# Kernel optimization log

Hardware: AMD Instinct MI355X
Metric: run time of the kernel (lower is better)

The kernel has to match this reference:

```python
import jax, jax.numpy as jnp
import numpy as np


def sparsemax(z):
    # sparsemax along the last axis (matches tfa.activations.sparsemax default axis=-1)
    K = z.shape[-1]
    zs = -jnp.sort(-z, axis=-1)                      # descending sort
    cs = jnp.cumsum(zs, axis=-1)
    k = jnp.arange(1, K + 1, dtype=z.dtype)
    support = 1.0 + k * zs > cs                      # support set indicator
    kmax = jnp.sum(support, axis=-1, keepdims=True)  # |support|, int
    cs_k = jnp.take_along_axis(cs, kmax - 1, axis=-1)
    tau = (cs_k - 1.0) / kmax.astype(z.dtype)
    return jnp.maximum(z - tau, 0.0)


def binary_lut(depth):
    # (depth, 2**depth, 2) table mapping leaf index -> per-level bit / complement
    idx = np.arange(2 ** depth)
    off = 2 ** np.arange(depth)
    bits = (idx[None, :] // off[:, None]) % 2        # (depth, 2**depth)
    return jnp.asarray(np.stack([bits, 1 - bits], axis=-1), dtype=jnp.float32)


def setup_inputs() -> dict:
    key = jax.random.key(0)
    ks = jax.random.split(key, 5)
    B, F, N, D, U = 8192, 256, 128, 6, 16
    return {
        "x": jax.random.normal(ks[0], (B, F), dtype=jnp.float32),
        "feature_selection_logits": jax.random.normal(ks[1], (F, N, D), dtype=jnp.float32),
        "feature_thresholds": jax.random.normal(ks[2], (N, D), dtype=jnp.float32),
        "log_temperatures": jax.random.normal(ks[3], (N, D), dtype=jnp.float32) * 0.1,
        "response": jax.random.normal(ks[4], (N, U, 2 ** D), dtype=jnp.float32),
        "depth": D,
    }


def reference(x, feature_selection_logits, feature_thresholds, log_temperatures, response, depth):
    lut = binary_lut(depth)                                          # (d, 2**d, 2)
    selectors = sparsemax(feature_selection_logits)                  # (i, n, d)
    fv = jnp.einsum('bi,ind->bnd', x, selectors)                     # (b, n, d)
    tl = (fv - feature_thresholds) * jnp.exp(-log_temperatures)      # (b, n, d)
    tl = jnp.stack([-tl, tl], axis=-1)                               # (b, n, d, 2)
    gates = jnp.clip(0.5 * tl + 0.5, 0.0, 1.0)                       # sparsemoid
    rg = jnp.einsum('bnds,dcs->bndc', gates, lut)                    # (b, n, d, 2**d)
    rg = jnp.prod(rg, axis=-2)                                       # (b, n, 2**d)
    resp = jnp.einsum('bnc,nuc->bnu', rg, response)                  # (b, n, u)
    return jnp.mean(resp, axis=1)                                    # (b, u)
```

## Files before the change

### kernel.cpp

```cpp
#include <hip/hip_runtime.h>


typedef float f32x4 __attribute__((ext_vector_type(4)));
typedef unsigned int u32;
typedef _Float16 h16;
typedef _Float16 h16x2 __attribute__((ext_vector_type(2)));
typedef _Float16 h16x8 __attribute__((ext_vector_type(8)));

typedef unsigned short __attribute__((may_alias)) u16a;
typedef u32            __attribute__((may_alias)) u32a;
typedef float          __attribute__((may_alias)) f32a;

#define WPF_OFF   0
#define RESPF_OFF 393216
#define BIAS_OFF  655360

union h2u { h16x2 h; u32 u; };
union hbits { h16 h; unsigned short s; };
union fragh { u32 w[4]; h16x8 v; int4 i4; h16x2 h2[4]; };

__device__ inline unsigned short h16r(float f) {
    hbits t; t.h = (h16)f; return t.s;
}
__device__ inline u32 packh2(float a, float b) {
    h2u t; t.h[0] = (h16)a; t.h[1] = (h16)b; return t.u;
}

__device__ inline f32x4 mfma_f16(h16x8 a, h16x8 b, f32x4 c) {
    return __builtin_amdgcn_mfma_f32_16x16x32_f16(a, b, c, 0, 0, 0);
}

__global__ __launch_bounds__(256) void k_prep(const float* __restrict__ fsl,
                                              const float* __restrict__ thr,
                                              const float* __restrict__ logt,
                                              const float* __restrict__ resp,
                                              unsigned short* __restrict__ WpF,
                                              unsigned short* __restrict__ respF,
                                              float* __restrict__ bias) {
    int bb  = blockIdx.x;
    int tid = threadIdx.x;
    if (bb < 128) {
        __shared__ unsigned short sm[8][192];
        int ib = (bb & 31) * 8;
        int nb = (bb >> 5) * 32;
        int il = tid >> 5;
        int nl = tid & 31;
        int i = ib + il;
        int n = nb + nl;
        const float* zp = fsl + (i * 128 + n) * 6;

        float z[6], zs[6];
        #pragma unroll
        for (int d = 0; d < 6; ++d) { z[d] = zp[d]; zs[d] = z[d]; }
        #pragma unroll
        for (int a = 0; a < 5; ++a) {
            #pragma unroll
            for (int b = a + 1; b < 6; ++b) {
                float hi = fmaxf(zs[a], zs[b]);
                float lo = fminf(zs[a], zs[b]);
                zs[a] = hi; zs[b] = lo;
            }
        }
        float cs = 0.f, csel = 0.f;
        int   km = 1;
        #pragma unroll
        for (int k = 0; k < 6; ++k) {
            cs += zs[k];
            if (1.0f + (float)(k + 1) * zs[k] > cs) { km = k + 1; csel = cs; }
        }
        float tau = (csel - 1.0f) / (float)km;

        #pragma unroll
        for (int d = 0; d < 6; ++d) {
            float invT = expf(-logt[n * 6 + d]);
            float sel  = fmaxf(z[d] - tau, 0.0f);
            float wv   = sel * 0.5f * invT;
            sm[il][nl * 6 + d] = h16r(wv);
            if (i == 0) bias[n * 6 + d] = 0.5f - 0.5f * invT * thr[n * 6 + d];
        }
        __syncthreads();

        if (tid < 192) {
            int ct  = (nb * 6) / 16 + (tid >> 4);
            int clm = tid & 15;
            int kt  = ib >> 5;
            int lq  = (ib >> 3) & 3;
            union { unsigned short s[8]; int4 i4; } o;
            #pragma unroll
            for (int j = 0; j < 8; ++j) o.s[j] = sm[j][tid];
            *(int4*)(WpF + (size_t)(((ct * 8 + kt) * 64 + lq * 16 + clm) * 8)) = o.i4;
        }
    } else {
        int t = (bb - 128) * 256 + tid;
        int n  = t >> 7;
        int k2 = (t >> 6) & 1;
        int l  = t & 63;
        int u  = l & 15;
        int c0 = k2 * 32 + (l >> 4) * 8;
        const float* rp = resp + n * 1024 + u * 64 + c0;
        float4 ra = *(const float4*)rp;
        float4 rb = *(const float4*)(rp + 4);
        int4 o;
        o.x = (int)packh2(ra.x, ra.y);
        o.y = (int)packh2(ra.z, ra.w);
        o.z = (int)packh2(rb.x, rb.y);
        o.w = (int)packh2(rb.z, rb.w);
        ((int4*)respF)[(n * 2 + k2) * 64 + l] = o;
    }
}

__global__ __launch_bounds__(1024, 4) void k_main(const float* __restrict__ x,
                                                  const unsigned short* __restrict__ WpF,
                                                  const unsigned short* __restrict__ respF,
                                                  const float* __restrict__ bias,
                                                  float* __restrict__ out) {
    __shared__ char smemraw[65536];
    const int4* xf4 = (const int4*)smemraw;

    int tid = threadIdx.x;
    int w  = tid >> 6;
    int l  = tid & 63;
    int cl = l & 15;
    int lq = l >> 4;
    int rowbase = blockIdx.x * 32;
    int ctbase  = w * 3;

    u16a* gw = (u16a*)(smemraw + 16384 + w * 3072);
    const int4* wp4 = (const int4*)WpF;
    const int4* rp4 = (const int4*)respF;

    {
        int k8  = tid & 31;
        int row = tid >> 5;
        const float* xp = x + (size_t)(rowbase + row) * 256 + k8 * 8;
        float4 xa = *(const float4*)(xp);
        float4 xb = *(const float4*)(xp + 4);
        int4 p;
        p.x = (int)packh2(xa.x, xa.y);
        p.y = (int)packh2(xa.z, xa.w);
        p.z = (int)packh2(xb.x, xb.y);
        p.w = (int)packh2(xb.z, xb.w);
        int rt = row >> 4, rl = row & 15, kt = k8 >> 2, klq = k8 & 3;
        char* basep = smemraw + (size_t)(rt * 8 + kt) * 1024
                              + (size_t)(((klq * 16 + rl) ^ kt) * 16);
        *(int4*)basep = p;
    }

    fragh bc[3];
    #pragma unroll
    for (int j = 0; j < 3; ++j)
        bc[j].i4 = wp4[((ctbase + j) * 8 + 0) * 64 + l];

    __syncthreads();

    f32x4 acc[3][2];
    #pragma unroll
    for (int j = 0; j < 3; ++j) {
        acc[j][0] = (f32x4){0.f, 0.f, 0.f, 0.f};
        acc[j][1] = (f32x4){0.f, 0.f, 0.f, 0.f};
    }

    #pragma unroll
    for (int kt = 0; kt < 8; ++kt) {
        fragh bn[3];
        if (kt < 7) {
            #pragma unroll
            for (int j = 0; j < 3; ++j)
                bn[j].i4 = wp4[((ctbase + j) * 8 + kt + 1) * 64 + l];
        }
        fragh ah0, ah1;
        ah0.i4 = xf4[(0 * 8 + kt) * 64 + (l ^ kt)];
        ah1.i4 = xf4[(1 * 8 + kt) * 64 + (l ^ kt)];
        #pragma unroll
        for (int j = 0; j < 3; ++j)
            acc[j][0] = mfma_f16(ah0.v, bc[j].v, acc[j][0]);
        #pragma unroll
        for (int j = 0; j < 3; ++j)
            acc[j][1] = mfma_f16(ah1.v, bc[j].v, acc[j][1]);
        if (kt < 7) {
            bc[0] = bn[0]; bc[1] = bn[1]; bc[2] = bn[2];
        }
    }

    fragh rc0, rc1;
    rc0.i4 = rp4[((w * 8 + 0) * 2 + 0) * 64 + l];
    rc1.i4 = rp4[((w * 8 + 0) * 2 + 1) * 64 + l];

    #pragma unroll
    for (int j = 0; j < 3; ++j) {
        int colg = (ctbase + j) * 16 + cl;
        int coll = j * 16 + cl;
        float bv = bias[colg];
        #pragma unroll
        for (int rt = 0; rt < 2; ++rt) {
            #pragma unroll
            for (int r = 0; r < 4; ++r) {
                float g = acc[j][rt][r] + bv;
                g = fminf(fmaxf(g, 0.f), 1.f);
                int row = rt * 16 + lq * 4 + r;
                gw[row * 48 + coll] = h16r(g);
            }
        }
    }

    f32x4 oacc0 = (f32x4){0.f, 0.f, 0.f, 0.f};
    f32x4 oacc1 = (f32x4){0.f, 0.f, 0.f, 0.f};
    const h16x2 onev = (h16x2){(h16)1.0f, (h16)1.0f};

    #pragma unroll
    for (int t2 = 0; t2 < 8; ++t2) {
        fragh rn0, rn1;
        if (t2 < 7) {
            rn0.i4 = rp4[((w * 8 + t2 + 1) * 2 + 0) * 64 + l];
            rn1.i4 = rp4[((w * 8 + t2 + 1) * 2 + 1) * 64 + l];
        }
        #pragma unroll
        for (int rt = 0; rt < 2; ++rt) {
            int row = rt * 16 + cl;
            const u32a* gp = (const u32a*)((const char*)gw + row * 96 + t2 * 12);
            h2u g01u, g23u, g45u;
            g01u.u = gp[0]; g23u.u = gp[1]; g45u.u = gp[2];
            h16x2 g01 = g01u.h, g23 = g23u.h, g45 = g45u.h;
            h16x2 s01 = onev - g01;
            h16x2 s23 = onev - g23;
            h16x2 s45 = onev - g45;
            h16x2 gs0  = __builtin_shufflevector(g01, s01, 0, 2);
            h16x2 b1g  = __builtin_shufflevector(g01, g01, 1, 1);
            h16x2 b1s  = __builtin_shufflevector(s01, s01, 1, 1);
            h16x2 t01a = gs0 * b1g;
            h16x2 t01b = gs0 * b1s;
            h16x2 g2b  = __builtin_shufflevector(g23, g23, 0, 0);
            h16x2 s2b  = __builtin_shufflevector(s23, s23, 0, 0);
            h16x2 pa01 = t01a * g2b;
            h16x2 pa23 = t01b * g2b;
            h16x2 pa45 = t01a * s2b;
            h16x2 pa67 = t01b * s2b;
            h16 f3  = (lq & 1) ? s23[1] : g23[1];
            h16 f4  = (lq & 2) ? s45[0] : g45[0];
            h16 m34 = f3 * f4;
            h16 pbl = m34 * g45[1];
            h16 pbh = m34 * s45[1];
            h16x2 pblb = (h16x2){pbl, pbl};
            h16x2 pbhb = (h16x2){pbh, pbh};
            fragh fa1, fa2;
            fa1.h2[0] = pa01 * pblb; fa1.h2[1] = pa23 * pblb;
            fa1.h2[2] = pa45 * pblb; fa1.h2[3] = pa67 * pblb;
            fa2.h2[0] = pa01 * pbhb; fa2.h2[1] = pa23 * pbhb;
            fa2.h2[2] = pa45 * pbhb; fa2.h2[3] = pa67 * pbhb;
            if (rt == 0) {
                oacc0 = mfma_f16(fa1.v, rc0.v, oacc0);
                oacc0 = mfma_f16(fa2.v, rc1.v, oacc0);
            } else {
                oacc1 = mfma_f16(fa1.v, rc0.v, oacc1);
                oacc1 = mfma_f16(fa2.v, rc1.v, oacc1);
            }
        }
        if (t2 < 7) { rc0 = rn0; rc1 = rn1; }
    }

    {
        f32a* pw = (f32a*)(smemraw + 16384 + w * 3072);
        int us = (cl + w) & 15;
        #pragma unroll
        for (int r = 0; r < 4; ++r) {
            pw[(lq * 4 + r) * 16 + us]        = oacc0[r];
            pw[(16 + lq * 4 + r) * 16 + us]   = oacc1[r];
        }
    }
    __syncthreads();

    if (tid < 512) {
        int r = tid >> 4, u = tid & 15;
        const f32a* pb = (const f32a*)(smemraw + 16384);
        float s = 0.f;
        #pragma unroll
        for (int ww = 0; ww < 16; ++ww)
            s += pb[ww * 768 + r * 16 + ((u + ww) & 15)];
        out[(size_t)(rowbase + r) * 16 + u] = s * (1.0f / 128.0f);
    }
}

extern "C" void kernel_launch(void* const* d_in, const int* in_sizes, int n_in,
                              void* d_out, int out_size, void* d_ws, size_t ws_size,
                              hipStream_t stream) {
    (void)in_sizes; (void)n_in; (void)out_size; (void)ws_size;
    const float* x    = (const float*)d_in[0];
    const float* fsl  = (const float*)d_in[1];
    const float* thr  = (const float*)d_in[2];
    const float* logt = (const float*)d_in[3];
    const float* resp = (const float*)d_in[4];

    char* ws = (char*)d_ws;
    unsigned short* WpF   = (unsigned short*)(ws + WPF_OFF);
    unsigned short* respF = (unsigned short*)(ws + RESPF_OFF);
    float*          bias  = (float*)(ws + BIAS_OFF);
    float* out = (float*)d_out;

    k_prep<<<192, 256, 0, stream>>>(fsl, thr, logt, resp, WpF, respF, bias);
    k_main<<<256, 1024, 0, stream>>>(x, WpF, respF, bias, out);
}
```

Before: 21.03 us.

## Enlarge prep blocks, pad gate LDS stride, relocate x tile, drop response prefetch

The prep kernel now runs as 48 blocks of 1024 threads instead of 192 of 256, and its logits and temperatures are read with vectorized float2 loads. In the main kernel the x tile moves to the top of shared memory. The per-wave gate buffer gets a padded 52-half stride to cut LDS bank conflicts, and a barrier is added before the gate writes because the regions now overlap. The response-product loop is split into an inlined helper that loads its response fragments directly rather than double-buffering them, which may expose global load latency in exchange for fewer live registers.

```diff
diff --git a/kernel.cpp b/kernel.cpp
--- a/kernel.cpp
+++ b/kernel.cpp
@@ -11,6 +11,11 @@
 typedef u32            __attribute__((may_alias)) u32a;
 typedef float          __attribute__((may_alias)) f32a;
 
+#define MEMFENCE asm volatile("" ::: "memory")
+
+#define GSTRIDE_U16 52
+#define GSLICE_B    3328
+
 #define WPF_OFF   0
 #define RESPF_OFF 393216
 #define BIAS_OFF  655360
@@ -30,28 +35,32 @@
     return __builtin_amdgcn_mfma_f32_16x16x32_f16(a, b, c, 0, 0, 0);
 }
 
-__global__ __launch_bounds__(256) void k_prep(const float* __restrict__ fsl,
-                                              const float* __restrict__ thr,
-                                              const float* __restrict__ logt,
-                                              const float* __restrict__ resp,
-                                              unsigned short* __restrict__ WpF,
-                                              unsigned short* __restrict__ respF,
-                                              float* __restrict__ bias) {
+__global__ __launch_bounds__(1024) void k_prep(const float* __restrict__ fsl,
+                                               const float* __restrict__ thr,
+                                               const float* __restrict__ logt,
+                                               const float* __restrict__ resp,
+                                               unsigned short* __restrict__ WpF,
+                                               unsigned short* __restrict__ respF,
+                                               float* __restrict__ bias) {
     int bb  = blockIdx.x;
     int tid = threadIdx.x;
-    if (bb < 128) {
-        __shared__ unsigned short sm[8][192];
-        int ib = (bb & 31) * 8;
-        int nb = (bb >> 5) * 32;
+    if (bb < 32) {
+        __shared__ unsigned short sm[32][192];
+        int ib = (bb & 7) * 32;
+        int nb = (bb >> 3) * 32;
         int il = tid >> 5;
         int nl = tid & 31;
         int i = ib + il;
         int n = nb + nl;
-        const float* zp = fsl + (i * 128 + n) * 6;
-
-        float z[6], zs[6];
-        #pragma unroll
-        for (int d = 0; d < 6; ++d) { z[d] = zp[d]; zs[d] = z[d]; }
+        const float* zp = fsl + (size_t)(i * 128 + n) * 6;
+
+        float2 za = *(const float2*)(zp);
+        float2 zb = *(const float2*)(zp + 2);
+        float2 zc = *(const float2*)(zp + 4);
+        float z[6] = {za.x, za.y, zb.x, zb.y, zc.x, zc.y};
+        float zs[6];
+        #pragma unroll
+        for (int d = 0; d < 6; ++d) zs[d] = z[d];
         #pragma unroll
         for (int a = 0; a < 5; ++a) {
             #pragma unroll
@@ -70,28 +79,35 @@
         }
         float tau = (csel - 1.0f) / (float)km;
 
+        const float* lp = logt + n * 6;
+        float2 la = *(const float2*)(lp);
+        float2 lb = *(const float2*)(lp + 2);
+        float2 lc = *(const float2*)(lp + 4);
+        float lt[6] = {la.x, la.y, lb.x, lb.y, lc.x, lc.y};
+
         #pragma unroll
         for (int d = 0; d < 6; ++d) {
-            float invT = expf(-logt[n * 6 + d]);
+            float invT = expf(-lt[d]);
             float sel  = fmaxf(z[d] - tau, 0.0f);
-            float wv   = sel * 0.5f * invT;
-            sm[il][nl * 6 + d] = h16r(wv);
+            sm[il][nl * 6 + d] = h16r(sel * 0.5f * invT);
             if (i == 0) bias[n * 6 + d] = 0.5f - 0.5f * invT * thr[n * 6 + d];
         }
         __syncthreads();
 
-        if (tid < 192) {
-            int ct  = (nb * 6) / 16 + (tid >> 4);
-            int clm = tid & 15;
-            int kt  = ib >> 5;
-            int lq  = (ib >> 3) & 3;
+        if (tid < 768) {
+            int lq  = tid / 192;
+            int rem = tid - lq * 192;
+            int ct  = (nb * 6) >> 4;
+            ct += rem >> 4;
+            int clm = rem & 15;
+            int kt  = bb & 7;
             union { unsigned short s[8]; int4 i4; } o;
             #pragma unroll
-            for (int j = 0; j < 8; ++j) o.s[j] = sm[j][tid];
+            for (int j = 0; j < 8; ++j) o.s[j] = sm[lq * 8 + j][rem];
             *(int4*)(WpF + (size_t)(((ct * 8 + kt) * 64 + lq * 16 + clm) * 8)) = o.i4;
         }
     } else {
-        int t = (bb - 128) * 256 + tid;
+        int t = (bb - 32) * 1024 + tid;
         int n  = t >> 7;
         int k2 = (t >> 6) & 1;
         int l  = t & 63;
@@ -109,13 +125,63 @@
     }
 }
 
+__device__ inline void pv_tree(const char* gwb, const int4* rp4, int n, int t2,
+                               int cl, int lq, int l, f32x4& o0, f32x4& o1) {
+    const h16x2 onev = (h16x2){(h16)1.0f, (h16)1.0f};
+    fragh rb0, rb1;
+    rb0.i4 = rp4[(n * 2 + 0) * 64 + l];
+    rb1.i4 = rp4[(n * 2 + 1) * 64 + l];
+    #pragma unroll
+    for (int rt = 0; rt < 2; ++rt) {
+        int row = rt * 16 + cl;
+        const u32a* gp = (const u32a*)(gwb + row * (GSTRIDE_U16 * 2) + t2 * 12);
+        h2u g01u, g23u, g45u;
+        g01u.u = gp[0]; g23u.u = gp[1]; g45u.u = gp[2];
+        h16x2 g01 = g01u.h, g23 = g23u.h, g45 = g45u.h;
+        h16x2 s01 = onev - g01;
+        h16x2 s23 = onev - g23;
+        h16x2 s45 = onev - g45;
+        h16x2 gs0  = __builtin_shufflevector(g01, s01, 0, 2);
+        h16x2 b1g  = __builtin_shufflevector(g01, g01, 1, 1);
+        h16x2 b1s  = __builtin_shufflevector(s01, s01, 1, 1);
+        h16x2 t01a = gs0 * b1g;
+        h16x2 t01b = gs0 * b1s;
+        h16x2 g2b  = __builtin_shufflevector(g23, g23, 0, 0);
+        h16x2 s2b  = __builtin_shufflevector(s23, s23, 0, 0);
+        h16x2 pa01 = t01a * g2b;
+        h16x2 pa23 = t01b * g2b;
+        h16x2 pa45 = t01a * s2b;
+        h16x2 pa67 = t01b * s2b;
+        h16 f3  = (lq & 1) ? s23[1] : g23[1];
+        h16 f4  = (lq & 2) ? s45[0] : g45[0];
+        h16 m34 = f3 * f4;
+        h16 pbl = m34 * g45[1];
+        h16 pbh = m34 * s45[1];
+        h16x2 pblb = (h16x2){pbl, pbl};
+        h16x2 pbhb = (h16x2){pbh, pbh};
+        fragh fa1, fa2;
+        fa1.h2[0] = pa01 * pblb; fa1.h2[1] = pa23 * pblb;
+        fa1.h2[2] = pa45 * pblb; fa1.h2[3] = pa67 * pblb;
+        fa2.h2[0] = pa01 * pbhb; fa2.h2[1] = pa23 * pbhb;
+        fa2.h2[2] = pa45 * pbhb; fa2.h2[3] = pa67 * pbhb;
+        if (rt == 0) {
+            o0 = mfma_f16(fa1.v, rb0.v, o0);
+            o0 = mfma_f16(fa2.v, rb1.v, o0);
+        } else {
+            o1 = mfma_f16(fa1.v, rb0.v, o1);
+            o1 = mfma_f16(fa2.v, rb1.v, o1);
+        }
+    }
+}
+
 __global__ __launch_bounds__(1024, 4) void k_main(const float* __restrict__ x,
                                                   const unsigned short* __restrict__ WpF,
                                                   const unsigned short* __restrict__ respF,
                                                   const float* __restrict__ bias,
                                                   float* __restrict__ out) {
     __shared__ char smemraw[65536];
-    const int4* xf4 = (const int4*)smemraw;
+    char* xfraw = smemraw + 49152;
+    const int4* xf4 = (const int4*)xfraw;
 
     int tid = threadIdx.x;
     int w  = tid >> 6;
@@ -125,7 +191,7 @@
     int rowbase = blockIdx.x * 32;
     int ctbase  = w * 3;
 
-    u16a* gw = (u16a*)(smemraw + 16384 + w * 3072);
+    char* gwb = smemraw + w * GSLICE_B;
     const int4* wp4 = (const int4*)WpF;
     const int4* rp4 = (const int4*)respF;
 
@@ -141,8 +207,8 @@
         p.z = (int)packh2(xb.x, xb.y);
         p.w = (int)packh2(xb.z, xb.w);
         int rt = row >> 4, rl = row & 15, kt = k8 >> 2, klq = k8 & 3;
-        char* basep = smemraw + (size_t)(rt * 8 + kt) * 1024
-                              + (size_t)(((klq * 16 + rl) ^ kt) * 16);
+        char* basep = xfraw + (size_t)(rt * 8 + kt) * 1024
+                            + (size_t)(((klq * 16 + rl) ^ kt) * 16);
         *(int4*)basep = p;
     }
 
@@ -150,6 +216,7 @@
     #pragma unroll
     for (int j = 0; j < 3; ++j)
         bc[j].i4 = wp4[((ctbase + j) * 8 + 0) * 64 + l];
+    MEMFENCE;
 
     __syncthreads();
 
@@ -168,98 +235,56 @@
             for (int j = 0; j < 3; ++j)
                 bn[j].i4 = wp4[((ctbase + j) * 8 + kt + 1) * 64 + l];
         }
-        fragh ah0, ah1;
-        ah0.i4 = xf4[(0 * 8 + kt) * 64 + (l ^ kt)];
-        ah1.i4 = xf4[(1 * 8 + kt) * 64 + (l ^ kt)];
+        fragh a0, a1;
+        a0.i4 = xf4[(0 * 8 + kt) * 64 + (l ^ kt)];
+        a1.i4 = xf4[(1 * 8 + kt) * 64 + (l ^ kt)];
         #pragma unroll
         for (int j = 0; j < 3; ++j)
-            acc[j][0] = mfma_f16(ah0.v, bc[j].v, acc[j][0]);
+            acc[j][0] = mfma_f16(a0.v, bc[j].v, acc[j][0]);
         #pragma unroll
         for (int j = 0; j < 3; ++j)
-            acc[j][1] = mfma_f16(ah1.v, bc[j].v, acc[j][1]);
-        if (kt < 7) {
-            bc[0] = bn[0]; bc[1] = bn[1]; bc[2] = bn[2];
-        }
+            acc[j][1] = mfma_f16(a1.v, bc[j].v, acc[j][1]);
+        if (kt < 7) { bc[0] = bn[0]; bc[1] = bn[1]; bc[2] = bn[2]; }
     }
 
     fragh rc0, rc1;
     rc0.i4 = rp4[((w * 8 + 0) * 2 + 0) * 64 + l];
     rc1.i4 = rp4[((w * 8 + 0) * 2 + 1) * 64 + l];
-
+    MEMFENCE;
+
+    __syncthreads();
+
+    u16a* gw16 = (u16a*)gwb;
     #pragma unroll
     for (int j = 0; j < 3; ++j) {
-        int colg = (ctbase + j) * 16 + cl;
-        int coll = j * 16 + cl;
-        float bv = bias[colg];
+        float bv = bias[(ctbase + j) * 16 + cl];
         #pragma unroll
         for (int rt = 0; rt < 2; ++rt) {
             #pragma unroll
             for (int r = 0; r < 4; ++r) {
                 float g = acc[j][rt][r] + bv;
                 g = fminf(fmaxf(g, 0.f), 1.f);
-                int row = rt * 16 + lq * 4 + r;
-                gw[row * 48 + coll] = h16r(g);
+                gw16[(rt * 16 + lq * 4 + r) * GSTRIDE_U16 + j * 16 + cl] = h16r(g);
             }
         }
     }
 
     f32x4 oacc0 = (f32x4){0.f, 0.f, 0.f, 0.f};
     f32x4 oacc1 = (f32x4){0.f, 0.f, 0.f, 0.f};
-    const h16x2 onev = (h16x2){(h16)1.0f, (h16)1.0f};
-
-    #pragma unroll
-    for (int t2 = 0; t2 < 8; ++t2) {
-        fragh rn0, rn1;
-        if (t2 < 7) {
-            rn0.i4 = rp4[((w * 8 + t2 + 1) * 2 + 0) * 64 + l];
-            rn1.i4 = rp4[((w * 8 + t2 + 1) * 2 + 1) * 64 + l];
-        }
-        #pragma unroll
-        for (int rt = 0; rt < 2; ++rt) {
-            int row = rt * 16 + cl;
-            const u32a* gp = (const u32a*)((const char*)gw + row * 96 + t2 * 12);
-            h2u g01u, g23u, g45u;
-            g01u.u = gp[0]; g23u.u = gp[1]; g45u.u = gp[2];
-            h16x2 g01 = g01u.h, g23 = g23u.h, g45 = g45u.h;
-            h16x2 s01 = onev - g01;
-            h16x2 s23 = onev - g23;
-            h16x2 s45 = onev - g45;
-            h16x2 gs0  = __builtin_shufflevector(g01, s01, 0, 2);
-            h16x2 b1g  = __builtin_shufflevector(g01, g01, 1, 1);
-            h16x2 b1s  = __builtin_shufflevector(s01, s01, 1, 1);
-            h16x2 t01a = gs0 * b1g;
-            h16x2 t01b = gs0 * b1s;
-            h16x2 g2b  = __builtin_shufflevector(g23, g23, 0, 0);
-            h16x2 s2b  = __builtin_shufflevector(s23, s23, 0, 0);
-            h16x2 pa01 = t01a * g2b;
-            h16x2 pa23 = t01b * g2b;
-            h16x2 pa45 = t01a * s2b;
-            h16x2 pa67 = t01b * s2b;
-            h16 f3  = (lq & 1) ? s23[1] : g23[1];
-            h16 f4  = (lq & 2) ? s45[0] : g45[0];
-            h16 m34 = f3 * f4;
-            h16 pbl = m34 * g45[1];
-            h16 pbh = m34 * s45[1];
-            h16x2 pblb = (h16x2){pbl, pbl};
-            h16x2 pbhb = (h16x2){pbh, pbh};
-            fragh fa1, fa2;
-            fa1.h2[0] = pa01 * pblb; fa1.h2[1] = pa23 * pblb;
-            fa1.h2[2] = pa45 * pblb; fa1.h2[3] = pa67 * pblb;
-            fa2.h2[0] = pa01 * pbhb; fa2.h2[1] = pa23 * pbhb;
-            fa2.h2[2] = pa45 * pbhb; fa2.h2[3] = pa67 * pbhb;
-            if (rt == 0) {
-                oacc0 = mfma_f16(fa1.v, rc0.v, oacc0);
-                oacc0 = mfma_f16(fa2.v, rc1.v, oacc0);
-            } else {
-                oacc1 = mfma_f16(fa1.v, rc0.v, oacc1);
-                oacc1 = mfma_f16(fa2.v, rc1.v, oacc1);
-            }
-        }
-        if (t2 < 7) { rc0 = rn0; rc1 = rn1; }
-    }
-
     {
-        f32a* pw = (f32a*)(smemraw + 16384 + w * 3072);
+        pv_tree(gwb, rp4, w * 8 + 0, 0, cl, lq, l, oacc0, oacc1);
+        pv_tree(gwb, rp4, w * 8 + 1, 1, cl, lq, l, oacc0, oacc1);
+        pv_tree(gwb, rp4, w * 8 + 2, 2, cl, lq, l, oacc0, oacc1);
+        pv_tree(gwb, rp4, w * 8 + 3, 3, cl, lq, l, oacc0, oacc1);
+        pv_tree(gwb, rp4, w * 8 + 4, 4, cl, lq, l, oacc0, oacc1);
+        pv_tree(gwb, rp4, w * 8 + 5, 5, cl, lq, l, oacc0, oacc1);
+        pv_tree(gwb, rp4, w * 8 + 6, 6, cl, lq, l, oacc0, oacc1);
+        pv_tree(gwb, rp4, w * 8 + 7, 7, cl, lq, l, oacc0, oacc1);
+        (void)rc0; (void)rc1;
+    }
+
+    {
+        f32a* pw = (f32a*)gwb;
         int us = (cl + w) & 15;
         #pragma unroll
         for (int r = 0; r < 4; ++r) {
@@ -271,11 +296,11 @@
 
     if (tid < 512) {
         int r = tid >> 4, u = tid & 15;
-        const f32a* pb = (const f32a*)(smemraw + 16384);
+        const f32a* pb = (const f32a*)smemraw;
         float s = 0.f;
         #pragma unroll
         for (int ww = 0; ww < 16; ++ww)
-            s += pb[ww * 768 + r * 16 + ((u + ww) & 15)];
+            s += pb[ww * (GSLICE_B / 4) + r * 16 + ((u + ww) & 15)];
         out[(size_t)(rowbase + r) * 16 + u] = s * (1.0f / 128.0f);
     }
 }
@@ -296,6 +321,6 @@
     float*          bias  = (float*)(ws + BIAS_OFF);
     float* out = (float*)d_out;
 
-    k_prep<<<192, 256, 0, stream>>>(fsl, thr, logt, resp, WpF, respF, bias);
+    k_prep<<<48, 1024, 0, stream>>>(fsl, thr, logt, resp, WpF, respF, bias);
     k_main<<<256, 1024, 0, stream>>>(x, WpF, respF, bias, out);
 }
```

After: 21.22 us. Within noise of the previous version (+0.9%).
